# Kernel tuning notes

Measured on AMD Instinct MI355X. Metric: run time of the kernel, lower is better.

## Reference

```python
import jax, jax.numpy as jnp
import numpy as np

B, C, H, W = 2, 256, 128, 128
S = 256          # num superpixels
QK = 256         # qk_dim
NUM_HEADS = 8
TOPK = 128
SCALE = (QK // NUM_HEADS) ** -0.5
EPS = 1e-5


def setup_inputs() -> dict:
    key = jax.random.key(0)
    k0, k1, k2, k3, k4 = jax.random.split(key, 5)
    x = jax.random.normal(k0, (B, C, H, W), jnp.float32)
    affinity_matrix = jax.random.normal(k1, (B, S, H * W), jnp.float32)
    wq = jax.random.normal(k2, (QK, C), jnp.float32) * 0.05
    wk = jax.random.normal(k3, (QK, C), jnp.float32) * 0.05
    wv = jax.random.normal(k4, (C, C), jnp.float32) * 0.05
    return {
        "x": x,
        "affinity_matrix": affinity_matrix,
        "ln_weight": jnp.ones((C,), jnp.float32),
        "ln_bias": jnp.zeros((C,), jnp.float32),
        "wq": wq,
        "wk": wk,
        "wv": wv,
        "num_spixels": S,
    }


def _forward(x, affinity_matrix, ln_weight, ln_bias, wq, wk, wv, num_spixels):
    Bx, Cx, Hx, Wx = x.shape
    HW = Hx * Wx
    h = NUM_HEADS
    T = TOPK
    Sx = num_spixels

    # LayerNorm2d: normalize over channel dim per pixel
    mu = x.mean(axis=1, keepdims=True)
    var = ((x - mu) ** 2).mean(axis=1, keepdims=True)
    xn = (x - mu) * jax.lax.rsqrt(var + EPS)
    xn = xn * ln_weight[None, :, None, None] + ln_bias[None, :, None, None]
    xf = xn.reshape(Bx, Cx, HW)

    # 1x1 convs as GEMMs: [out_ch, in_ch] x [B, in_ch, HW]
    q = jnp.einsum('oc,bcn->bon', wq, xf)   # [B, QK, HW]
    k = jnp.einsum('oc,bcn->bon', wk, xf)   # [B, QK, HW]
    v = jnp.einsum('oc,bcn->bon', wv, xf)   # [B, C,  HW]

    # top-k pixels per superpixel
    sims, indices = jax.lax.top_k(affinity_matrix, T)  # [B, S, T]

    def gath(t):  # t [B, D, HW] -> [B, D, S, T]
        return jax.vmap(lambda tb, ib: tb[:, ib])(t, indices)

    def heads(t):  # [B, D, S, T] -> [B, S, h, T, D//h]
        D = t.shape[1]
        return t.reshape(Bx, h, D // h, Sx, T).transpose(0, 3, 1, 4, 2)

    qh = heads(gath(q))  # [B,S,h,T,cq]
    kh = heads(gath(k))
    vh = heads(gath(v))  # [B,S,h,T,cv]

    attn = jnp.einsum('bshtc,bshuc->bshtu', qh, kh) * SCALE
    attn = jax.nn.softmax(attn, axis=-1)

    w = sims[:, :, None, :, None]            # [B,S,1,T,1]
    vw = vh * w                               # kweight=True
    out = jnp.einsum('bshtu,bshuc->bshtc', attn, vw)

    # 'b k h t c -> b (h c) (k t)'
    out = out.transpose(0, 2, 4, 1, 3).reshape(Bx, Cx, Sx * T)
    out = out * sims.reshape(Bx, 1, Sx * T)  # weight is broadcast over channels

    idx = indices.reshape(Bx, Sx * T)
    # weighted_scatter_mean with normz=False: tgt is v itself (not zeros)
    res = jax.vmap(lambda vb, ib, sb: vb.at[:, ib].add(sb))(v, idx, out)
    return res.reshape(Bx, Cx, Hx, Wx)


def reference(x, affinity_matrix, ln_weight, ln_bias, wq, wk, wv, num_spixels):
    return _forward(x, affinity_matrix, ln_weight, ln_bias, wq, wk, wv, num_spixels)
```

## Files before the change

kernel.cpp:

```cpp
#include <hip/hip_runtime.h>

#define HW      16384
#define C_DIM   256
#define S_DIM   256
#define T_K     128
#define NH      8
#define DH      32
#define QKV_ST  768
#define B_DIM   2
#define SCALE_F 0.17677669529663687f
#define CAND    1536
#define EQCAP   512
#define NROWS   (S_DIM * T_K)

typedef __attribute__((ext_vector_type(8))) short short8;
typedef __attribute__((ext_vector_type(4))) float f32x4;

__device__ __forceinline__ short f2bf(float f) {
    unsigned u = __float_as_uint(f);
    unsigned r = (u + 0x7FFFu + ((u >> 16) & 1u)) >> 16;
    return (short)r;
}
__device__ __forceinline__ float bf2f(short s) {
    unsigned u = ((unsigned)(unsigned short)s) << 16;
    return __uint_as_float(u);
}

__device__ __forceinline__ unsigned sortkey(float f) {
    unsigned u = __float_as_uint(f);
    return (u & 0x80000000u) ? ~u : (u | 0x80000000u);
}
__device__ __forceinline__ float keyval(unsigned k) {
    return __uint_as_float((k & 0x80000000u) ? (k ^ 0x80000000u) : ~k);
}

__launch_bounds__(256)
__global__ void ln_stats_kernel(const float* __restrict__ x,
                                float* __restrict__ mu,
                                float* __restrict__ rsig) {
    int q = threadIdx.x >> 6;
    int l = threadIdx.x & 63;
    int p = blockIdx.x * 64 + l;
    int b = p >> 14;
    int n = p & (HW - 1);
    const float* xb = x + (size_t)b * C_DIM * HW + n;
    float s = 0.f, ss = 0.f;
#pragma unroll 8
    for (int c = q * 64; c < q * 64 + 64; c++) {
        float v = xb[(size_t)c * HW];
        s += v; ss += v * v;
    }
    __shared__ float ps[4][64], pss[4][64];
    ps[q][l] = s; pss[q][l] = ss;
    __syncthreads();
    if (threadIdx.x < 64) {
        float S  = ps[0][l] + ps[1][l] + ps[2][l] + ps[3][l];
        float SS = pss[0][l] + pss[1][l] + pss[2][l] + pss[3][l];
        float m   = S * (1.f / C_DIM);
        float var = fmaxf(SS * (1.f / C_DIM) - m * m, 0.f);
        int pp = blockIdx.x * 64 + l;
        mu[pp]   = m;
        rsig[pp] = rsqrtf(var + 1e-5f);
    }
}

__global__ void wpack_kernel(const float* __restrict__ wq,
                             const float* __restrict__ wk,
                             const float* __restrict__ wv,
                             short* __restrict__ wb) {
    int gid  = blockIdx.x * 256 + threadIdx.x;
    int base = gid * 4;
    int o = base >> 8;
    int c = base & 255;
    const float* src = (o < 256) ? wq + (size_t)o * 256
                     : (o < 512) ? wk + (size_t)(o - 256) * 256
                                 : wv + (size_t)(o - 512) * 256;
    float4 w4 = *(const float4*)(src + c);
    short4 s4;
    s4.x = f2bf(w4.x); s4.y = f2bf(w4.y); s4.z = f2bf(w4.z); s4.w = f2bf(w4.w);
    *(short4*)&wb[base] = s4;
}

__launch_bounds__(256)
__global__ void xpack_kernel(const float* __restrict__ x,
                             const float* __restrict__ g,
                             const float* __restrict__ beta,
                             const float* __restrict__ mu,
                             const float* __restrict__ rsig,
                             short* __restrict__ xnT) {
    int b  = blockIdx.z;
    int n0 = blockIdx.x * 64;
    int c0 = blockIdx.y * 64;
    int tid = threadIdx.x;

    __shared__ float t[64][65];

    {
        int cl = tid >> 2;
        int ni = (tid & 3) * 16;
        const float* src = x + ((size_t)b * C_DIM + c0 + cl) * HW + n0 + ni;
#pragma unroll
        for (int j = 0; j < 4; j++) {
            float4 v = *(const float4*)(src + j * 4);
            t[cl][ni + j * 4 + 0] = v.x;
            t[cl][ni + j * 4 + 1] = v.y;
            t[cl][ni + j * 4 + 2] = v.z;
            t[cl][ni + j * 4 + 3] = v.w;
        }
    }
    __syncthreads();

    {
        int nl = tid >> 2;
        int ci = (tid & 3) * 16;
        int n  = n0 + nl;
        float m  = mu[b * HW + n];
        float rs = rsig[b * HW + n];
        short8 s0, s1;
#pragma unroll
        for (int j = 0; j < 8; j++) {
            int c = c0 + ci + j;
            s0[j] = f2bf((t[ci + j][nl] - m) * rs * g[c] + beta[c]);
        }
#pragma unroll
        for (int j = 0; j < 8; j++) {
            int c = c0 + ci + 8 + j;
            s1[j] = f2bf((t[ci + 8 + j][nl] - m) * rs * g[c] + beta[c]);
        }
        short* dst = xnT + ((size_t)b * HW + n) * C_DIM + c0 + ci;
        *(short8*)(dst)     = s0;
        *(short8*)(dst + 8) = s1;
    }
}

#define E_STRIDE 136
__launch_bounds__(256)
__global__ void qkv_mfma_kernel(const short* __restrict__ xnT,
                                const short* __restrict__ wb,
                                short* __restrict__ qkv) {
    int b  = blockIdx.z;
    int n0 = blockIdx.x * 128;
    int o0 = blockIdx.y * 128;
    int tid  = threadIdx.x;
    int wv   = tid >> 6;
    int wn   = wv & 1;
    int wo   = wv >> 1;
    int lane = tid & 63;
    int quad = lane >> 4;
    int ln   = lane & 15;

    __shared__ __align__(16) short Es[64 * E_STRIDE];

    const short* arow[4];
    const short* brow[4];
#pragma unroll
    for (int mt = 0; mt < 4; mt++)
        arow[mt] = xnT + ((size_t)b * HW + n0 + wn * 64 + mt * 16 + ln) * C_DIM + quad * 8;
#pragma unroll
    for (int nt = 0; nt < 4; nt++)
        brow[nt] = wb + (size_t)(o0 + wo * 64 + nt * 16 + ln) * C_DIM + quad * 8;

    f32x4 acc[4][4];
    const f32x4 zero4 = {0.f, 0.f, 0.f, 0.f};
#pragma unroll
    for (int mt = 0; mt < 4; mt++)
#pragma unroll
        for (int nt = 0; nt < 4; nt++) acc[mt][nt] = zero4;

#pragma unroll 2
    for (int c0 = 0; c0 < C_DIM; c0 += 32) {
        short8 af[4], bf[4];
#pragma unroll
        for (int mt = 0; mt < 4; mt++) af[mt] = *(const short8*)(arow[mt] + c0);
#pragma unroll
        for (int nt = 0; nt < 4; nt++) bf[nt] = *(const short8*)(brow[nt] + c0);
#pragma unroll
        for (int mt = 0; mt < 4; mt++)
#pragma unroll
            for (int nt = 0; nt < 4; nt++)
                acc[mt][nt] = __builtin_amdgcn_mfma_f32_16x16x32_bf16(af[mt], bf[nt], acc[mt][nt], 0, 0, 0);
    }

#pragma unroll
    for (int p = 0; p < 2; p++) {
        if (wn == p) {
#pragma unroll
            for (int mt = 0; mt < 4; mt++)
#pragma unroll
                for (int nt = 0; nt < 4; nt++)
#pragma unroll
                    for (int r = 0; r < 4; r++)
                        Es[(mt * 16 + quad * 4 + r) * E_STRIDE + wo * 64 + nt * 16 + ln] =
                            f2bf(acc[mt][nt][r]);
        }
        __syncthreads();
        {
            int nl = tid >> 2;
            int qo = (tid & 3) * 32;
            const short* srcr = &Es[nl * E_STRIDE + qo];
            short* dst = qkv + ((size_t)b * HW + n0 + p * 64 + nl) * QKV_ST + o0 + qo;
#pragma unroll
            for (int j = 0; j < 4; j++)
                *(short8*)(dst + j * 8) = *(const short8*)(srcr + j * 8);
        }
        __syncthreads();
    }
}

__launch_bounds__(1024)
__global__ void topk_kernel(const float* __restrict__ aff,
                            float* __restrict__ sims,
                            int* __restrict__ idx) {
    int s = blockIdx.x, b = blockIdx.y;
    int tid = threadIdx.x;
    const float4* rowv4 = (const float4*)(aff + ((size_t)b * S_DIM + s) * HW);

    __shared__ unsigned hist[256];
    __shared__ unsigned sufs[256];
    __shared__ unsigned ckey[CAND];
    __shared__ int      cidx[CAND];
    __shared__ int      eqix[EQCAP];
    __shared__ int s_sel, cHi, cCand, cEq;

    if (tid == 0) { cHi = 0; cCand = 0; cEq = 0; }
    if (tid < 256) hist[tid] = 0;
    __syncthreads();

    for (int i = tid; i < HW / 4; i += 1024) {
        float4 v = rowv4[i];
        atomicAdd(&hist[sortkey(v.x) >> 24], 1u);
        atomicAdd(&hist[sortkey(v.y) >> 24], 1u);
        atomicAdd(&hist[sortkey(v.z) >> 24], 1u);
        atomicAdd(&hist[sortkey(v.w) >> 24], 1u);
    }
    __syncthreads();

    if (tid < 256) sufs[tid] = hist[tid];
    __syncthreads();
#pragma unroll
    for (int off = 1; off < 256; off <<= 1) {
        unsigned v = 0;
        if (tid < 256 && tid + off < 256) v = sufs[tid + off];
        __syncthreads();
        if (tid < 256) sufs[tid] += v;
        __syncthreads();
    }

    int kneed = T_K;
    if (tid < 256) {
        unsigned above = (tid < 255) ? sufs[tid + 1] : 0u;
        if ((int)sufs[tid] >= kneed && (int)above < kneed) s_sel = tid;
    }
    __syncthreads();
    int sel = s_sel;
    unsigned prefix = (unsigned)sel << 24;
    kneed -= (int)((sel < 255) ? sufs[sel + 1] : 0u);
    __syncthreads();

    float* so = sims + ((size_t)b * S_DIM + s) * T_K;
    int*   io = idx  + ((size_t)b * S_DIM + s) * T_K;

    for (int i = tid; i < HW / 4; i += 1024) {
        float4 v = rowv4[i];
        float vf[4] = {v.x, v.y, v.z, v.w};
#pragma unroll
        for (int j = 0; j < 4; j++) {
            unsigned u  = sortkey(vf[j]);
            unsigned hb = u >> 24;
            if (hb > (unsigned)sel) {
                int p = atomicAdd(&cHi, 1);
                so[p] = vf[j]; io[p] = i * 4 + j;
            } else if (hb == (unsigned)sel) {
                int c = atomicAdd(&cCand, 1);
                if (c < CAND) { ckey[c] = u; cidx[c] = i * 4 + j; }
            }
        }
    }
    __syncthreads();
    int nc = min(cCand, CAND);

    for (int shift = 16; shift >= 0; shift -= 8) {
        if (tid < 256) hist[tid] = 0;
        __syncthreads();
        unsigned mask = 0xFFFFFFFFu << (shift + 8);
        for (int i = tid; i < nc; i += 1024) {
            unsigned u = ckey[i];
            if ((u & mask) == prefix) atomicAdd(&hist[(u >> shift) & 255], 1u);
        }
        __syncthreads();
        if (tid < 256) sufs[tid] = hist[tid];
        __syncthreads();
#pragma unroll
        for (int off = 1; off < 256; off <<= 1) {
            unsigned v = 0;
            if (tid < 256 && tid + off < 256) v = sufs[tid + off];
            __syncthreads();
            if (tid < 256) sufs[tid] += v;
            __syncthreads();
        }
        if (tid < 256) {
            unsigned above = (tid < 255) ? sufs[tid + 1] : 0u;
            if ((int)sufs[tid] >= kneed && (int)above < kneed) s_sel = tid;
        }
        __syncthreads();
        sel = s_sel;
        prefix |= (unsigned)sel << shift;
        kneed  -= (int)((sel < 255) ? sufs[sel + 1] : 0u);
        __syncthreads();
    }

    unsigned T = prefix;
    int kneedF = kneed;

    for (int i = tid; i < nc; i += 1024) {
        unsigned u = ckey[i];
        if (u > T) {
            int p = atomicAdd(&cHi, 1);
            so[p] = keyval(u); io[p] = cidx[i];
        } else if (u == T) {
            int q = atomicAdd(&cEq, 1);
            if (q < EQCAP) eqix[q] = cidx[i];
        }
    }
    __syncthreads();
    int m = min(cEq, EQCAP);

    float tval = keyval(T);
    for (int i = tid; i < m; i += 1024) {
        int my = eqix[i];
        int rank = 0;
        for (int j = 0; j < m; j++) rank += (eqix[j] < my);
        if (rank < kneedF) { so[127 - rank] = tval; io[127 - rank] = my; }
    }
}

__global__ void count_kernel(const int* __restrict__ idx,
                             int* __restrict__ cnt) {
    int b = blockIdx.y;
    int i = blockIdx.x * 256 + threadIdx.x;
    int n = idx[(size_t)b * NROWS + i];
    atomicAdd(&cnt[b * HW + n], 1);
}

__launch_bounds__(1024)
__global__ void scan_kernel(const int* __restrict__ cnt,
                            int* __restrict__ offs) {
    int b = blockIdx.x;
    const int* c = cnt + b * HW;
    int* o = offs + b * HW;
    int tid = threadIdx.x;
    __shared__ int part[1024];
    int base = tid * 16;
    int loc[16];
    int s = 0;
#pragma unroll
    for (int j = 0; j < 16; j++) { loc[j] = s; s += c[base + j]; }
    part[tid] = s;
    __syncthreads();
    for (int off = 1; off < 1024; off <<= 1) {
        int v = (tid >= off) ? part[tid - off] : 0;
        __syncthreads();
        part[tid] += v;
        __syncthreads();
    }
    int pre = (tid == 0) ? 0 : part[tid - 1];
#pragma unroll
    for (int j = 0; j < 16; j++) o[base + j] = pre + loc[j];
}

__global__ void fill_kernel(const int* __restrict__ idx,
                            const int* __restrict__ offs,
                            int* __restrict__ fcnt,
                            int* __restrict__ slots) {
    int b = blockIdx.y;
    int i = blockIdx.x * 256 + threadIdx.x;
    int n = idx[(size_t)b * NROWS + i];
    int r = atomicAdd(&fcnt[b * HW + n], 1);
    slots[(size_t)b * NROWS + offs[b * HW + n] + r] = i;
}

#define K_STRIDE 40
#define VT_STRIDE 132
union KPu {
    short K[T_K * K_STRIDE];
    short P[4][16 * VT_STRIDE];
};
__launch_bounds__(256)
__global__ void attn_kernel(const short* __restrict__ qkv,
                            const float* __restrict__ sims,
                            const int* __restrict__ idx,
                            float* __restrict__ dout) {
    int s = blockIdx.x, h = blockIdx.y, b = blockIdx.z;
    int tid  = threadIdx.x;
    int wv   = tid >> 6;
    int lane = tid & 63;
    int quad = lane >> 4;
    int ln   = lane & 15;

    __shared__ __align__(16) KPu KP;
    __shared__ __align__(16) short Vt[DH * VT_STRIDE];
    __shared__ float sim_s[T_K];
    __shared__ int   idx_s[T_K];

    if (tid < T_K) {
        sim_s[tid] = sims[((size_t)b * S_DIM + s) * T_K + tid];
        idx_s[tid] = idx [((size_t)b * S_DIM + s) * T_K + tid];
    }
    __syncthreads();

    const short* qkvb = qkv + (size_t)b * HW * QKV_ST;
    int co = h * DH;

    {
        int r  = tid >> 1;
        int hh = tid & 1;
        const short* base = qkvb + (size_t)idx_s[r] * QKV_ST + co + hh * 16;
        short8 k0 = *(const short8*)(base + 256);
        short8 k1 = *(const short8*)(base + 256 + 8);
        *(short8*)&KP.K[r * K_STRIDE + hh * 16]     = k0;
        *(short8*)&KP.K[r * K_STRIDE + hh * 16 + 8] = k1;
        short8 v0 = *(const short8*)(base + 512);
        short8 v1 = *(const short8*)(base + 512 + 8);
#pragma unroll
        for (int i = 0; i < 8; i++) Vt[(hh * 16 + i) * VT_STRIDE + r]     = v0[i];
#pragma unroll
        for (int i = 0; i < 8; i++) Vt[(hh * 16 + 8 + i) * VT_STRIDE + r] = v1[i];
    }

    short8 aq[2];
#pragma unroll
    for (int mt = 0; mt < 2; mt++) {
        int t = wv * 32 + mt * 16 + ln;
        aq[mt] = *(const short8*)(qkvb + (size_t)idx_s[t] * QKV_ST + co + quad * 8);
    }
    __syncthreads();

    f32x4 S[2][8];
    const f32x4 zero4 = {0.f, 0.f, 0.f, 0.f};
    __builtin_amdgcn_s_setprio(1);
#pragma unroll
    for (int nt = 0; nt < 8; nt++) {
        short8 kf = *(const short8*)&KP.K[(nt * 16 + ln) * K_STRIDE + quad * 8];
        S[0][nt] = __builtin_amdgcn_mfma_f32_16x16x32_bf16(aq[0], kf, zero4, 0, 0, 0);
        S[1][nt] = __builtin_amdgcn_mfma_f32_16x16x32_bf16(aq[1], kf, zero4, 0, 0, 0);
    }
    __builtin_amdgcn_s_setprio(0);

    float lrow[2][4];
#pragma unroll
    for (int mt = 0; mt < 2; mt++) {
#pragma unroll
        for (int r = 0; r < 4; r++) {
            float mx = S[mt][0][r];
#pragma unroll
            for (int nt = 1; nt < 8; nt++) mx = fmaxf(mx, S[mt][nt][r]);
            mx = fmaxf(mx, __shfl_xor(mx, 1, 64));
            mx = fmaxf(mx, __shfl_xor(mx, 2, 64));
            mx = fmaxf(mx, __shfl_xor(mx, 4, 64));
            mx = fmaxf(mx, __shfl_xor(mx, 8, 64));
            float l = 0.f;
#pragma unroll
            for (int nt = 0; nt < 8; nt++) {
                float p = __expf((S[mt][nt][r] - mx) * SCALE_F);
                S[mt][nt][r] = p;
                l += p;
            }
            l += __shfl_xor(l, 1, 64);
            l += __shfl_xor(l, 2, 64);
            l += __shfl_xor(l, 4, 64);
            l += __shfl_xor(l, 8, 64);
            lrow[mt][r] = l;
        }
    }

    __syncthreads();

    float* db = dout + ((size_t)b * NROWS + s * T_K) * C_DIM + co;
#pragma unroll
    for (int mt = 0; mt < 2; mt++) {
        float w[4];
#pragma unroll
        for (int r = 0; r < 4; r++)
            w[r] = sim_s[wv * 32 + mt * 16 + quad * 4 + r] / lrow[mt][r];

#pragma unroll
        for (int nt = 0; nt < 8; nt++) {
            float su = sim_s[nt * 16 + ln];
#pragma unroll
            for (int r = 0; r < 4; r++)
                KP.P[wv][(quad * 4 + r) * VT_STRIDE + nt * 16 + ln] = f2bf(S[mt][nt][r] * su);
        }

        f32x4 O[2] = {zero4, zero4};
        __builtin_amdgcn_s_setprio(1);
#pragma unroll
        for (int kt = 0; kt < 4; kt++) {
            short8 pa = *(const short8*)&KP.P[wv][ln * VT_STRIDE + kt * 32 + quad * 8];
#pragma unroll
            for (int nt2 = 0; nt2 < 2; nt2++) {
                short8 vb = *(const short8*)&Vt[(nt2 * 16 + ln) * VT_STRIDE + kt * 32 + quad * 8];
                O[nt2] = __builtin_amdgcn_mfma_f32_16x16x32_bf16(pa, vb, O[nt2], 0, 0, 0);
            }
        }
        __builtin_amdgcn_s_setprio(0);

#pragma unroll
        for (int nt2 = 0; nt2 < 2; nt2++)
#pragma unroll
            for (int r = 0; r < 4; r++) {
                int t = wv * 32 + mt * 16 + quad * 4 + r;
                db[(size_t)t * C_DIM + nt2 * 16 + ln] = O[nt2][r] * w[r];
            }
    }
}

__launch_bounds__(256)
__global__ void transpose_add_kernel(const short* __restrict__ qkv,
                                     const float* __restrict__ dout,
                                     const int* __restrict__ cnt,
                                     const int* __restrict__ offs,
                                     const int* __restrict__ slots,
                                     float* __restrict__ out) {
    int b  = blockIdx.z;
    int n0 = blockIdx.x * 32;
    int c0 = blockIdx.y * 128;
    int x4 = threadIdx.x & 31;
    int y  = threadIdx.x >> 5;

    const float* doutb = dout + (size_t)b * NROWS * C_DIM;
    const int*   slb   = slots + (size_t)b * NROWS;

    __shared__ float t[32][129];

#pragma unroll
    for (int r = 0; r < 4; r++) {
        int px = y + 8 * r;
        int n  = n0 + px;
        size_t row = (size_t)b * HW + n;
        short4 vs = *(const short4*)(qkv + row * QKV_ST + 512 + c0 + x4 * 4);
        float a0 = bf2f(vs.x), a1 = bf2f(vs.y), a2 = bf2f(vs.z), a3 = bf2f(vs.w);
        int cn = cnt[b * HW + n];
        int of = offs[b * HW + n];
        for (int j = 0; j < cn; j++) {
            int dr = slb[of + j];
            float4 d = *(const float4*)(doutb + (size_t)dr * C_DIM + c0 + x4 * 4);
            a0 += d.x; a1 += d.y; a2 += d.z; a3 += d.w;
        }
        t[px][x4 * 4 + 0] = a0;
        t[px][x4 * 4 + 1] = a1;
        t[px][x4 * 4 + 2] = a2;
        t[px][x4 * 4 + 3] = a3;
    }
    __syncthreads();

    {
        int nl = threadIdx.x & 31;
        int cg = threadIdx.x >> 5;
#pragma unroll
        for (int cc = 0; cc < 16; cc++) {
            int c = c0 + cg * 16 + cc;
            out[((size_t)b * C_DIM + c) * HW + n0 + nl] = t[nl][cg * 16 + cc];
        }
    }
}

extern "C" void kernel_launch(void* const* d_in, const int* in_sizes, int n_in,
                              void* d_out, int out_size, void* d_ws, size_t ws_size,
                              hipStream_t stream) {
    const float* x    = (const float*)d_in[0];
    const float* aff  = (const float*)d_in[1];
    const float* g    = (const float*)d_in[2];
    const float* beta = (const float*)d_in[3];
    const float* wq   = (const float*)d_in[4];
    const float* wk   = (const float*)d_in[5];
    const float* wv   = (const float*)d_in[6];
    float* out = (float*)d_out;

    char* ws = (char*)d_ws;
    short* qkv  = (short*)ws;                                   ws += (size_t)B_DIM * HW * QKV_ST * 2;
    short* xnT  = (short*)ws;                                   ws += (size_t)B_DIM * HW * C_DIM * 2;
    short* wbuf = (short*)ws;                                   ws += (size_t)QKV_ST * C_DIM * 2;
    float* mu   = (float*)ws;                                   ws += (size_t)B_DIM * HW * 4;
    float* rsig = (float*)ws;                                   ws += (size_t)B_DIM * HW * 4;
    float* simsb= (float*)ws;                                   ws += (size_t)B_DIM * S_DIM * T_K * 4;
    int*   idxb = (int*)ws;                                     ws += (size_t)B_DIM * S_DIM * T_K * 4;
    int*   cntb = (int*)ws;                                     ws += (size_t)B_DIM * HW * 4;
    int*   offsb= (int*)ws;                                     ws += (size_t)B_DIM * HW * 4;
    int*   fcnt = (int*)ws;                                     ws += (size_t)B_DIM * HW * 4;
    int*   slots= (int*)ws;                                     ws += (size_t)B_DIM * NROWS * 4;
    float* dout = (float*)ws;

    hipMemsetAsync(cntb, 0, (size_t)B_DIM * HW * sizeof(int), stream);
    hipMemsetAsync(fcnt, 0, (size_t)B_DIM * HW * sizeof(int), stream);

    ln_stats_kernel<<<dim3(B_DIM * HW / 64), 256, 0, stream>>>(x, mu, rsig);
    wpack_kernel<<<dim3(QKV_ST * C_DIM / 4 / 256), 256, 0, stream>>>(wq, wk, wv, wbuf);
    xpack_kernel<<<dim3(HW / 64, C_DIM / 64, B_DIM), 256, 0, stream>>>(
        x, g, beta, mu, rsig, xnT);
    qkv_mfma_kernel<<<dim3(HW / 128, QKV_ST / 128, B_DIM), 256, 0, stream>>>(
        xnT, wbuf, qkv);
    topk_kernel<<<dim3(S_DIM, B_DIM), 1024, 0, stream>>>(aff, simsb, idxb);
    count_kernel<<<dim3(NROWS / 256, B_DIM), 256, 0, stream>>>(idxb, cntb);
    scan_kernel<<<dim3(B_DIM), 1024, 0, stream>>>(cntb, offsb);
    fill_kernel<<<dim3(NROWS / 256, B_DIM), 256, 0, stream>>>(idxb, offsb, fcnt, slots);
    attn_kernel<<<dim3(S_DIM, NH, B_DIM), 256, 0, stream>>>(qkv, simsb, idxb, dout);
    transpose_add_kernel<<<dim3(HW / 32, C_DIM / 128, B_DIM), 256, 0, stream>>>(
        qkv, dout, cntb, offsb, slots, out);
}
```

Measured before the change: 290.0 us.

## Stage QKV GEMM tiles through double-buffered LDS with register prefetch

```diff
diff --git a/kernel.cpp b/kernel.cpp
--- a/kernel.cpp
+++ b/kernel.cpp
@@ -134,6 +134,7 @@
 }
 
 #define E_STRIDE 136
+#define A_STR   36
 __launch_bounds__(256)
 __global__ void qkv_mfma_kernel(const short* __restrict__ xnT,
                                 const short* __restrict__ wb,
@@ -149,16 +150,27 @@
     int quad = lane >> 4;
     int ln   = lane & 15;
 
-    __shared__ __align__(16) short Es[64 * E_STRIDE];
-
-    const short* arow[4];
-    const short* brow[4];
+    __shared__ __align__(16) union {
+        short S[2][2][128 * A_STR];
+        short Es[64 * E_STRIDE];
+    } L;
+
+    int r1 = tid >> 2,        q1 = tid & 3;
+    int r2 = (tid + 256) >> 2, q2 = (tid + 256) & 3;
+    const short* gA1 = xnT + ((size_t)b * HW + n0 + r1) * C_DIM + q1 * 8;
+    const short* gA2 = xnT + ((size_t)b * HW + n0 + r2) * C_DIM + q2 * 8;
+    const short* gB1 = wb + (size_t)(o0 + r1) * C_DIM + q1 * 8;
+    const short* gB2 = wb + (size_t)(o0 + r2) * C_DIM + q2 * 8;
+    int la1 = r1 * A_STR + q1 * 8;
+    int la2 = r2 * A_STR + q2 * 8;
+
+    int aoff[4], boff[4];
 #pragma unroll
     for (int mt = 0; mt < 4; mt++)
-        arow[mt] = xnT + ((size_t)b * HW + n0 + wn * 64 + mt * 16 + ln) * C_DIM + quad * 8;
+        aoff[mt] = (wn * 64 + mt * 16 + ln) * A_STR + quad * 8;
 #pragma unroll
     for (int nt = 0; nt < 4; nt++)
-        brow[nt] = wb + (size_t)(o0 + wo * 64 + nt * 16 + ln) * C_DIM + quad * 8;
+        boff[nt] = (wo * 64 + nt * 16 + ln) * A_STR + quad * 8;
 
     f32x4 acc[4][4];
     const f32x4 zero4 = {0.f, 0.f, 0.f, 0.f};
@@ -167,18 +179,50 @@
 #pragma unroll
         for (int nt = 0; nt < 4; nt++) acc[mt][nt] = zero4;
 
+    {
+        short8 ra1 = *(const short8*)gA1;
+        short8 ra2 = *(const short8*)gA2;
+        short8 rb1 = *(const short8*)gB1;
+        short8 rb2 = *(const short8*)gB2;
+        *(short8*)&L.S[0][0][la1] = ra1;
+        *(short8*)&L.S[0][0][la2] = ra2;
+        *(short8*)&L.S[0][1][la1] = rb1;
+        *(short8*)&L.S[0][1][la2] = rb2;
+    }
+    __syncthreads();
+
 #pragma unroll 2
-    for (int c0 = 0; c0 < C_DIM; c0 += 32) {
+    for (int t = 0; t < 8; t++) {
+        int cur = t & 1;
+        short8 ra1, ra2, rb1, rb2;
+        if (t < 7) {
+            int c0 = (t + 1) * 32;
+            ra1 = *(const short8*)(gA1 + c0);
+            ra2 = *(const short8*)(gA2 + c0);
+            rb1 = *(const short8*)(gB1 + c0);
+            rb2 = *(const short8*)(gB2 + c0);
+        }
+
         short8 af[4], bf[4];
 #pragma unroll
-        for (int mt = 0; mt < 4; mt++) af[mt] = *(const short8*)(arow[mt] + c0);
-#pragma unroll
-        for (int nt = 0; nt < 4; nt++) bf[nt] = *(const short8*)(brow[nt] + c0);
+        for (int mt = 0; mt < 4; mt++) af[mt] = *(const short8*)&L.S[cur][0][aoff[mt]];
+#pragma unroll
+        for (int nt = 0; nt < 4; nt++) bf[nt] = *(const short8*)&L.S[cur][1][boff[nt]];
+        __builtin_amdgcn_s_setprio(1);
 #pragma unroll
         for (int mt = 0; mt < 4; mt++)
 #pragma unroll
             for (int nt = 0; nt < 4; nt++)
                 acc[mt][nt] = __builtin_amdgcn_mfma_f32_16x16x32_bf16(af[mt], bf[nt], acc[mt][nt], 0, 0, 0);
+        __builtin_amdgcn_s_setprio(0);
+
+        if (t < 7) {
+            *(short8*)&L.S[cur ^ 1][0][la1] = ra1;
+            *(short8*)&L.S[cur ^ 1][0][la2] = ra2;
+            *(short8*)&L.S[cur ^ 1][1][la1] = rb1;
+            *(short8*)&L.S[cur ^ 1][1][la2] = rb2;
+        }
+        __syncthreads();
     }
 
 #pragma unroll
@@ -190,14 +234,14 @@
                 for (int nt = 0; nt < 4; nt++)
 #pragma unroll
                     for (int r = 0; r < 4; r++)
-                        Es[(mt * 16 + quad * 4 + r) * E_STRIDE + wo * 64 + nt * 16 + ln] =
+                        L.Es[(mt * 16 + quad * 4 + r) * E_STRIDE + wo * 64 + nt * 16 + ln] =
                             f2bf(acc[mt][nt][r]);
         }
         __syncthreads();
         {
             int nl = tid >> 2;
             int qo = (tid & 3) * 32;
-            const short* srcr = &Es[nl * E_STRIDE + qo];
+            const short* srcr = &L.Es[nl * E_STRIDE + qo];
             short* dst = qkv + ((size_t)b * HW + n0 + p * 64 + nl) * QKV_ST + o0 + qo;
 #pragma unroll
             for (int j = 0; j < 4; j++)
```

After: 268.9 us. 7.3% less time.
